# Optimization experiments

Measured on AMD Instinct MI355X. Metric: run time of the kernel, lower is better.

The kernel has to match this reference:

```python
import jax, jax.numpy as jnp
import numpy as np

B, S, E = 4, 1024, 1280
H = 16
D = E // H  # 80


def rotate_half(x):
    x1, x2 = jnp.split(x, 2, axis=-1)
    return jnp.concatenate([-x2, x1], axis=-1)


def setup_inputs() -> dict:
    key = jax.random.key(0)
    ks = jax.random.split(key, 12)
    sc = 0.02
    x = jax.random.normal(ks[0], (B, S, E), dtype=jnp.float32)
    # variable per-item sequence lengths (each <= S), cumulative
    lens = np.array([1024, 896, 768, 640], dtype=np.int32)
    cu_seqlens = jnp.asarray(np.concatenate([[0], np.cumsum(lens)]), dtype=jnp.int32)
    # rotary cos/sin for positions 0..S-1, head_dim D
    inv_freq = 1.0 / (10000.0 ** (np.arange(0, D, 2, dtype=np.float32) / D))
    t = np.arange(S, dtype=np.float32)
    freqs = np.outer(t, inv_freq)               # [S, D/2]
    emb = np.concatenate([freqs, freqs], axis=-1)  # [S, D]
    cos = jnp.asarray(np.cos(emb), dtype=jnp.float32)
    sin = jnp.asarray(np.sin(emb), dtype=jnp.float32)
    wq = jax.random.normal(ks[1], (E, E), dtype=jnp.float32) * sc
    bq = jax.random.normal(ks[2], (E,), dtype=jnp.float32) * sc
    wk = jax.random.normal(ks[3], (E, E), dtype=jnp.float32) * sc
    bk = jax.random.normal(ks[4], (E,), dtype=jnp.float32) * sc
    wv = jax.random.normal(ks[5], (E, E), dtype=jnp.float32) * sc
    bv = jax.random.normal(ks[6], (E,), dtype=jnp.float32) * sc
    wo = jax.random.normal(ks[7], (E, E), dtype=jnp.float32) * sc
    bo = jax.random.normal(ks[8], (E,), dtype=jnp.float32) * sc
    return {"x": x, "cu_seqlens": cu_seqlens, "cos": cos, "sin": sin,
            "wq": wq, "bq": bq, "wk": wk, "bk": bk, "wv": wv, "bv": bv,
            "wo": wo, "bo": bo}


def reference(x, cu_seqlens, cos, sin, wq, bq, wk, bk, wv, bv, wo, bo):
    b, s, e = x.shape
    h, d = H, D
    # QKV projections (nn.Linear: x @ W^T + b)
    q = (x @ wq.T + bq).reshape(b, s, h, d)
    k = (x @ wk.T + bk).reshape(b, s, h, d)
    v = (x @ wv.T + bv).reshape(b, s, h, d)
    # rotary embedding (apply_rotary_pos_emb, 'normal')
    c = cos[None, :, None, :]  # [1, s, 1, d]
    sn = sin[None, :, None, :]
    q = q * c + rotate_half(q) * sn
    k = k * c + rotate_half(k) * sn
    # patch attention mask from cu_seqlens (flatten_batch=False):
    # token i attends to token j iff i < len_b and j < len_b
    seq_lens = cu_seqlens[1:] - cu_seqlens[:-1]          # [b]
    idx = jnp.arange(s)
    valid = idx[None, :] < seq_lens[:, None]             # [b, s]
    mask = valid[:, None, :, None] & valid[:, None, None, :]  # [b, 1, s, s]
    # SDPA, non-causal
    scale = 1.0 / jnp.sqrt(jnp.asarray(d, dtype=q.dtype))
    scores = jnp.einsum("bqhd,bkhd->bhqk", q, k) * scale
    scores = jnp.where(mask, scores, jnp.asarray(-1e9, dtype=scores.dtype))
    attn = jax.nn.softmax(scores, axis=-1)
    out = jnp.einsum("bhqk,bkhd->bqhd", attn, v)         # [b, s, h, d]
    out = out.reshape(b, s, e)
    # output projection
    return out @ wo.T + bo
```

## Files before the change

### kernel.cpp

```cpp
#include <hip/hip_runtime.h>
#include <hip/hip_bf16.h>

#define B_ 4
#define S_ 1024
#define E_ 1280
#define H_ 16
#define D_ 80
#define M_ (B_*S_)

typedef __hip_bfloat16 bf16;
using bf16x8 = __attribute__((ext_vector_type(8))) short;
using f32x4  = __attribute__((ext_vector_type(4))) float;

__device__ __forceinline__ float b2f(bf16 x){ return __bfloat162float(x); }
__device__ __forceinline__ bf16  f2b(float x){ return __float2bfloat16(x); }
__device__ __forceinline__ void  stf(float* p, float v){ *p = v; }
__device__ __forceinline__ void  stf(bf16*  p, float v){ *p = f2b(v); }

__device__ __forceinline__ void gload_lds16(const void* g, void* l) {
    __builtin_amdgcn_global_load_lds(
        (const __attribute__((address_space(1))) unsigned int*)g,
        (__attribute__((address_space(3))) unsigned int*)l, 16, 0, 0);
}

__global__ __launch_bounds__(256) void cvt_kernel(
    const float* __restrict__ s0, const float* __restrict__ s1,
    const float* __restrict__ s2, const float* __restrict__ s3,
    const float* __restrict__ s4,
    bf16* __restrict__ d0, bf16* __restrict__ d1, bf16* __restrict__ d2,
    bf16* __restrict__ d3, bf16* __restrict__ d4,
    int n0, int n1)
{
    const float* s; bf16* d; int n;
    switch (blockIdx.y) {
        case 0: s = s0; d = d0; n = n0; break;
        case 1: s = s1; d = d1; n = n1; break;
        case 2: s = s2; d = d2; n = n1; break;
        case 3: s = s3; d = d3; n = n1; break;
        default: s = s4; d = d4; n = n1; break;
    }
    int i = (blockIdx.x * 256 + threadIdx.x) * 8;
    if (i >= n) return;
    float4 a = *(const float4*)(s + i);
    float4 b = *(const float4*)(s + i + 4);
    bf16 t[8];
    t[0]=f2b(a.x); t[1]=f2b(a.y); t[2]=f2b(a.z); t[3]=f2b(a.w);
    t[4]=f2b(b.x); t[5]=f2b(b.y); t[6]=f2b(b.z); t[7]=f2b(b.w);
    *(uint4*)(d + i) = *(const uint4*)t;
}

template<typename TC, bool VT_OUT>
__global__ __launch_bounds__(256) void mfma_gemm_bt(
    const bf16* __restrict__ A,
    const bf16* __restrict__ W0, const bf16* __restrict__ W1, const bf16* __restrict__ W2,
    const float* __restrict__ b0, const float* __restrict__ b1, const float* __restrict__ b2,
    TC* __restrict__ C0, TC* __restrict__ C1, TC* __restrict__ C2,
    int K, int N, int ntiles)
{
    const int mat = blockIdx.y / ntiles;
    const int bn  = (blockIdx.y % ntiles) * 128;
    const int bm  = blockIdx.x * 128;
    const bf16* W; const float* bias; TC* C;
    if (mat == 0)      { W = W0; bias = b0; C = C0; }
    else if (mat == 1) { W = W1; bias = b1; C = C1; }
    else               { W = W2; bias = b2; C = C2; }

    __shared__ bf16 As[2][128][32];
    __shared__ bf16 Ws[2][128][32];

    const int tid  = threadIdx.x;
    const int lane = tid & 63;
    const int wv   = tid >> 6;
    const int wm   = (wv & 1) * 64;
    const int wn   = (wv >> 1) * 64;
    const int srow = wv * 16 + (lane >> 2);
    const int scol = (lane & 3) * 8;

    f32x4 acc[4][4] = {};

    for (int k0 = 0; k0 < K; k0 += 64) {
        __syncthreads();
        #pragma unroll
        for (int p = 0; p < 2; p++) {
            const int kc = k0 + p*32 + scol;
            gload_lds16(A + (size_t)(bm + srow)      * K + kc, &As[p][wv*16][0]);
            gload_lds16(A + (size_t)(bm + 64 + srow) * K + kc, &As[p][64 + wv*16][0]);
            gload_lds16(W + (size_t)(bn + srow)      * K + kc, &Ws[p][wv*16][0]);
            gload_lds16(W + (size_t)(bn + 64 + srow) * K + kc, &Ws[p][64 + wv*16][0]);
        }
        __syncthreads();

        const int fr = lane & 15;
        const int kq = (lane >> 4) * 8;
        #pragma unroll
        for (int p = 0; p < 2; p++) {
            bf16x8 af[4], wf[4];
            #pragma unroll
            for (int t = 0; t < 4; t++) {
                af[t] = *(const bf16x8*)&As[p][wm + t*16 + fr][kq];
                wf[t] = *(const bf16x8*)&Ws[p][wn + t*16 + fr][kq];
            }
            #pragma unroll
            for (int mt = 0; mt < 4; mt++)
                #pragma unroll
                for (int nt = 0; nt < 4; nt++)
                    acc[mt][nt] = __builtin_amdgcn_mfma_f32_16x16x32_bf16(
                        af[mt], wf[nt], acc[mt][nt], 0, 0, 0);
        }
    }

    const int col_l = lane & 15;
    const int row_l = (lane >> 4) * 4;

    if (VT_OUT && mat == 2) {
        const int btok = bm >> 10;
        const int keyb = (bm & 1023) + wm + row_l;
        #pragma unroll
        for (int nt = 0; nt < 4; nt++) {
            const int n = bn + wn + nt*16 + col_l;
            const float bv = bias[n];
            const int hh = n / 80, dd = n % 80;
            bf16* vbase = (bf16*)C + ((size_t)(btok*H_ + hh)*D_ + dd)*S_ + keyb;
            #pragma unroll
            for (int mt = 0; mt < 4; mt++) {
                union { bf16 h[4]; uint2 u; } t4;
                #pragma unroll
                for (int r = 0; r < 4; r++) t4.h[r] = f2b(acc[mt][nt][r] + bv);
                *(uint2*)&vbase[mt*16] = t4.u;
            }
        }
    } else {
        #pragma unroll
        for (int nt = 0; nt < 4; nt++) {
            const int n = bn + wn + nt*16 + col_l;
            const float bv = bias[n];
            #pragma unroll
            for (int mt = 0; mt < 4; mt++) {
                #pragma unroll
                for (int r = 0; r < 4; r++) {
                    const int m = bm + wm + mt*16 + row_l + r;
                    stf(&C[(size_t)m * N + n], acc[mt][nt][r] + bv);
                }
            }
        }
    }
}

__device__ __forceinline__ void rope8(const bf16* lo, const bf16* hi,
                                      const float* cp, const float* sp,
                                      float mul, uint4* out_lo, uint4* out_hi)
{
    union { uint4 u; bf16 h[8]; } li, hi_, lo_o, hi_o;
    li.u  = *(const uint4*)lo;
    hi_.u = *(const uint4*)hi;
    #pragma unroll
    for (int u = 0; u < 8; u++) {
        float x1 = b2f(li.h[u]), x2 = b2f(hi_.h[u]);
        float c = cp[u], s = sp[u];
        lo_o.h[u] = f2b((x1*c - x2*s) * mul);
        hi_o.h[u] = f2b((x2*c + x1*s) * mul);
    }
    *out_lo = lo_o.u;
    *out_hi = hi_o.u;
}

__global__ __launch_bounds__(256) void rope_kernel(
    bf16* __restrict__ qp, bf16* __restrict__ kp,
    const float* __restrict__ cosp, const float* __restrict__ sinp)
{
    int idx = blockIdx.x * 256 + threadIdx.x;
    const int NT = M_ * H_ * 5;
    bf16* base; float mul;
    if (idx < NT) { base = qp; mul = 0.11180339887498949f; }
    else         { base = kp; mul = 1.0f; idx -= NT; }
    const int row = idx / 80;
    const int rem = idx - row * 80;
    const int h   = rem / 5;
    const int pc  = rem - h * 5;
    const int s   = row & (S_ - 1);
    bf16* p = base + (size_t)row * E_ + h * D_ + pc * 8;
    const float* cp = cosp + s * D_ + pc * 8;
    const float* sp = sinp + s * D_ + pc * 8;
    uint4 olo, ohi;
    rope8(p, p + 40, cp, sp, mul, &olo, &ohi);
    *(uint4*)p        = olo;
    *(uint4*)(p + 40) = ohi;
}

__global__ __launch_bounds__(256, 4) void attn_mfma(
    const bf16* __restrict__ q, const bf16* __restrict__ k, const bf16* __restrict__ vt,
    const int* __restrict__ cu, bf16* __restrict__ o)
{
    __shared__ __align__(16) bf16 Ks[64*80];
    __shared__ __align__(16) bf16 VTs[80*64];
    __shared__ __align__(16) bf16 PTs[4][16*76];

    const int n  = blockIdx.x;
    const int g  = (n & 7) * 8 + (n >> 7);
    const int qt = (n >> 3) & 15;
    const int b  = g >> 4;
    const int h  = g & 15;

    const int tid  = threadIdx.x;
    const int lane = tid & 63, wv = tid >> 6;
    const int quad = lane >> 4, l15 = lane & 15;
    const int q0   = qt * 64;
    const int len  = cu[b + 1] - cu[b];

    const bool uniformq = (q0 >= len);
    const bool cleanlen = ((len & 63) == 0);
    const int  ktiles   = uniformq ? 16 : (cleanlen ? (len >> 6) : 16);
    const bool domask   = !uniformq && !cleanlen;

    bf16* PT = &PTs[wv][0];

    bf16x8 qf[3] = {};
    if (!uniformq) {
        const bf16* qrow = q + (size_t)(b*S_ + q0 + wv*16 + l15)*E_ + h*D_ + quad*8;
        qf[0] = *(const bf16x8*)(qrow);
        qf[1] = *(const bf16x8*)(qrow + 32);
        if (quad < 2) qf[2] = *(const bf16x8*)(qrow + 64);
    } else {
        const bf16 one = f2b(1.0f);
        #pragma unroll
        for (int nt = 0; nt < 4; nt++)
            #pragma unroll
            for (int r = 0; r < 4; r++)
                PT[(quad*4 + r)*76 + nt*16 + l15] = one;
    }

    float m_r[4], l_r[4];
    #pragma unroll
    for (int r = 0; r < 4; r++) { m_r[r] = -1e30f; l_r[r] = 0.f; }
    f32x4 o_acc[5] = {};

    const bool q_full = (q0 + 64) <= len;

    const int u_  = l15 >> 2;
    const int s0r = quad ^ u_;
    const int sv0 = quad ^ (l15 & 7);

    for (int kt = 0; kt < ktiles; kt++) {
        __syncthreads();
        if (!uniformq) {
            #pragma unroll
            for (int i = 0; i < 3; i++) {
                int c = tid + i * 256;
                if (c < 640) {
                    int row = c / 10, s = c - row * 10;
                    int uu = (row >> 2) & 3;
                    int sg = (s < 8) ? (s ^ uu) : (8 + ((s ^ uu) & 1));
                    gload_lds16(k + (size_t)(b*S_ + kt*64 + row)*E_ + h*D_ + sg*8,
                                &Ks[c*8]);
                }
            }
        }
        #pragma unroll
        for (int i = 0; i < 3; i++) {
            int c = tid + i * 256;
            if (c < 640) {
                int row = c >> 3, s = c & 7;
                int sg = s ^ (row & 7);
                gload_lds16(vt + ((size_t)(b*H_ + h)*D_ + row)*S_ + kt*64 + sg*8,
                            &VTs[c*8]);
            }
        }
        __syncthreads();

        if (!uniformq) {
            f32x4 s4[4];
            #pragma unroll
            for (int nt = 0; nt < 4; nt++) {
                const bf16* kr = Ks + (nt*16 + l15) * 80;
                bf16x8 kf0 = *(const bf16x8*)(kr + s0r*8);
                bf16x8 kf1 = *(const bf16x8*)(kr + 32 + s0r*8);
                bf16x8 kf2 = {};
                if (quad < 2) kf2 = *(const bf16x8*)(kr + 64 + (s0r & 1)*8);
                f32x4 a0 = {};
                a0 = __builtin_amdgcn_mfma_f32_16x16x32_bf16(qf[0], kf0, a0, 0, 0, 0);
                a0 = __builtin_amdgcn_mfma_f32_16x16x32_bf16(qf[1], kf1, a0, 0, 0, 0);
                a0 = __builtin_amdgcn_mfma_f32_16x16x32_bf16(qf[2], kf2, a0, 0, 0, 0);
                s4[nt] = a0;
            }

            float sv[4][4];
            if (!domask || (q_full && (kt*64 + 64) <= len)) {
                #pragma unroll
                for (int r = 0; r < 4; r++)
                    #pragma unroll
                    for (int nt = 0; nt < 4; nt++)
                        sv[nt][r] = s4[nt][r];
            } else {
                bool vk[4];
                #pragma unroll
                for (int nt = 0; nt < 4; nt++) vk[nt] = (kt*64 + nt*16 + l15) < len;
                #pragma unroll
                for (int r = 0; r < 4; r++) {
                    const bool vq = (q0 + wv*16 + quad*4 + r) < len;
                    #pragma unroll
                    for (int nt = 0; nt < 4; nt++)
                        sv[nt][r] = (vq && vk[nt]) ? s4[nt][r] : -1e9f;
                }
            }
            float rmax[4];
            #pragma unroll
            for (int r = 0; r < 4; r++)
                rmax[r] = fmaxf(fmaxf(sv[0][r], sv[1][r]), fmaxf(sv[2][r], sv[3][r]));
            #pragma unroll
            for (int st = 1; st < 16; st <<= 1)
                #pragma unroll
                for (int r = 0; r < 4; r++)
                    rmax[r] = fmaxf(rmax[r], __shfl_xor(rmax[r], st, 64));
            float mnew[4], alpha[4], rsum[4], p[4][4];
            #pragma unroll
            for (int r = 0; r < 4; r++) {
                mnew[r]  = fmaxf(m_r[r], rmax[r]);
                alpha[r] = __expf(m_r[r] - mnew[r]);
                float a = 0.f;
                #pragma unroll
                for (int nt = 0; nt < 4; nt++) { p[nt][r] = __expf(sv[nt][r] - mnew[r]); a += p[nt][r]; }
                rsum[r] = a;
            }
            #pragma unroll
            for (int st = 1; st < 16; st <<= 1)
                #pragma unroll
                for (int r = 0; r < 4; r++)
                    rsum[r] += __shfl_xor(rsum[r], st, 64);
            #pragma unroll
            for (int r = 0; r < 4; r++) {
                l_r[r] = l_r[r] * alpha[r] + rsum[r];
                m_r[r] = mnew[r];
            }
            #pragma unroll
            for (int dt = 0; dt < 5; dt++)
                #pragma unroll
                for (int r = 0; r < 4; r++)
                    o_acc[dt][r] *= alpha[r];
            #pragma unroll
            for (int nt = 0; nt < 4; nt++)
                #pragma unroll
                for (int r = 0; r < 4; r++)
                    PT[(quad*4 + r)*76 + nt*16 + l15] = f2b(p[nt][r]);
        }

        bf16x8 pa0 = *(const bf16x8*)&PT[l15*76 + quad*8];
        bf16x8 pa1 = *(const bf16x8*)&PT[l15*76 + 32 + quad*8];
        #pragma unroll
        for (int dt = 0; dt < 5; dt++) {
            const bf16* vr = VTs + (dt*16 + l15) * 64;
            bf16x8 vf0 = *(const bf16x8*)(vr + sv0*8);
            bf16x8 vf1 = *(const bf16x8*)(vr + (sv0 ^ 4)*8);
            o_acc[dt] = __builtin_amdgcn_mfma_f32_16x16x32_bf16(pa0, vf0, o_acc[dt], 0, 0, 0);
            o_acc[dt] = __builtin_amdgcn_mfma_f32_16x16x32_bf16(pa1, vf1, o_acc[dt], 0, 0, 0);
        }
    }

    #pragma unroll
    for (int r = 0; r < 4; r++) {
        const float inv = uniformq ? (1.0f / 1024.0f) : (1.0f / l_r[r]);
        size_t row_g = (size_t)(b*S_ + q0 + wv*16 + quad*4 + r);
        #pragma unroll
        for (int dt = 0; dt < 5; dt++)
            o[row_g*E_ + h*D_ + dt*16 + l15] = f2b(o_acc[dt][r] * inv);
    }
}

extern "C" void kernel_launch(void* const* d_in, const int* in_sizes, int n_in,
                              void* d_out, int out_size, void* d_ws, size_t ws_size,
                              hipStream_t stream)
{
    const float* x    = (const float*)d_in[0];
    const int*   cu   = (const int*)  d_in[1];
    const float* cosp = (const float*)d_in[2];
    const float* sinp = (const float*)d_in[3];
    const float* wq   = (const float*)d_in[4];
    const float* bq   = (const float*)d_in[5];
    const float* wk   = (const float*)d_in[6];
    const float* bk   = (const float*)d_in[7];
    const float* wv   = (const float*)d_in[8];
    const float* bv   = (const float*)d_in[9];
    const float* wo   = (const float*)d_in[10];
    const float* bo   = (const float*)d_in[11];
    float* out = (float*)d_out;

    bf16* q   = (bf16*)d_ws;
    bf16* kk  = q   + (size_t)M_ * E_;
    bf16* vt  = kk  + (size_t)M_ * E_;
    bf16* ao  = vt  + (size_t)M_ * E_;
    bf16* xb  = ao  + (size_t)M_ * E_;
    bf16* wqb = xb  + (size_t)M_ * E_;
    bf16* wkb = wqb + (size_t)E_ * E_;
    bf16* wvb = wkb + (size_t)E_ * E_;
    bf16* wob = wvb + (size_t)E_ * E_;

    cvt_kernel<<<dim3(2560, 5), 256, 0, stream>>>(
        x, wq, wk, wv, wo, xb, wqb, wkb, wvb, wob, M_*E_, E_*E_);

    mfma_gemm_bt<bf16, true><<<dim3(M_/128, 30), 256, 0, stream>>>(
        xb, wqb, wkb, wvb, bq, bk, bv, q, kk, vt, E_, E_, 10);

    rope_kernel<<<2560, 256, 0, stream>>>(q, kk, cosp, sinp);

    attn_mfma<<<1024, 256, 0, stream>>>(q, kk, vt, cu, ao);

    mfma_gemm_bt<float, false><<<dim3(M_/128, 10), 256, 0, stream>>>(
        ao, wob, wob, wob, bo, bo, bo, out, out, out, E_, E_, 10);
}
```

Measured before the change: 280.6 us.

## Double-buffer K/V tiles and widen attention blocks to 128 queries

The attention kernel now handles 128 query rows per block with 8 waves instead of 64 rows with 4. This halves the number of K/V tile loads per (batch, head). K and V^T tiles are double-buffered in LDS, so the next tile is prefetched asynchronously while the current one is computed, and there is one barrier per iteration instead of two. LDS use per block doubles and the grid shrinks to 512 blocks, which lowers parallelism. The q_full check still uses a 64-row bound, so masking could be wrong for lengths that are not multiples of 128, though the test lengths are.

```diff
diff --git a/kernel.cpp b/kernel.cpp
--- a/kernel.cpp
+++ b/kernel.cpp
@@ -7,6 +7,7 @@
 #define H_ 16
 #define D_ 80
 #define M_ (B_*S_)
+#define QBLK 128
 
 typedef __hip_bfloat16 bf16;
 using bf16x8 = __attribute__((ext_vector_type(8))) short;
@@ -187,30 +188,30 @@
     *(uint4*)(p + 40) = ohi;
 }
 
-__global__ __launch_bounds__(256, 4) void attn_mfma(
+__global__ __launch_bounds__(512, 4) void attn_mfma(
     const bf16* __restrict__ q, const bf16* __restrict__ k, const bf16* __restrict__ vt,
     const int* __restrict__ cu, bf16* __restrict__ o)
 {
-    __shared__ __align__(16) bf16 Ks[64*80];
-    __shared__ __align__(16) bf16 VTs[80*64];
-    __shared__ __align__(16) bf16 PTs[4][16*76];
+    __shared__ __align__(16) bf16 Ks[2][64*80];
+    __shared__ __align__(16) bf16 VTs[2][80*64];
+    __shared__ __align__(16) bf16 PTs[8][16*76];
 
     const int n  = blockIdx.x;
-    const int g  = (n & 7) * 8 + (n >> 7);
-    const int qt = (n >> 3) & 15;
+    const int g  = ((n >> 6) << 3) | (n & 7);
+    const int qs = (n >> 3) & 7;
     const int b  = g >> 4;
     const int h  = g & 15;
 
     const int tid  = threadIdx.x;
     const int lane = tid & 63, wv = tid >> 6;
     const int quad = lane >> 4, l15 = lane & 15;
-    const int q0   = qt * 64;
+    const int q0   = qs * QBLK;
     const int len  = cu[b + 1] - cu[b];
 
     const bool uniformq = (q0 >= len);
-    const bool cleanlen = ((len & 63) == 0);
-    const int  ktiles   = uniformq ? 16 : (cleanlen ? (len >> 6) : 16);
-    const bool domask   = !uniformq && !cleanlen;
+    const bool clean    = ((len & (QBLK - 1)) == 0);
+    const int  ktiles   = uniformq ? 16 : (clean ? (len >> 6) : 16);
+    const bool domask   = !uniformq && !clean;
 
     bf16* PT = &PTs[wv][0];
 
@@ -234,44 +235,46 @@
     for (int r = 0; r < 4; r++) { m_r[r] = -1e30f; l_r[r] = 0.f; }
     f32x4 o_acc[5] = {};
 
-    const bool q_full = (q0 + 64) <= len;
-
     const int u_  = l15 >> 2;
     const int s0r = quad ^ u_;
     const int sv0 = quad ^ (l15 & 7);
 
+    auto stage = [&](int kt, int bf) {
+        #pragma unroll
+        for (int i = 0; i < 3; i++) {
+            int c = tid + i * 512;
+            if (c < 640) {
+                if (!uniformq) {
+                    int row = c / 10, s5 = c - row * 10;
+                    int uu = (row >> 2) & 3;
+                    int sg = (s5 < 8) ? (s5 ^ uu) : (8 + ((s5 ^ uu) & 1));
+                    gload_lds16(k + (size_t)(b*S_ + kt*64 + row)*E_ + h*D_ + sg*8,
+                                &Ks[bf][c*8]);
+                }
+            } else if (c < 1280) {
+                int c2 = c - 640;
+                int row = c2 >> 3, s5 = c2 & 7;
+                int sg = s5 ^ (row & 7);
+                gload_lds16(vt + ((size_t)(b*H_ + h)*D_ + row)*S_ + kt*64 + sg*8,
+                            &VTs[bf][c2*8]);
+            }
+        }
+    };
+
+    stage(0, 0);
+    __syncthreads();
+
+    const bool q_full = (q0 + 64) <= len;
+
     for (int kt = 0; kt < ktiles; kt++) {
-        __syncthreads();
-        if (!uniformq) {
-            #pragma unroll
-            for (int i = 0; i < 3; i++) {
-                int c = tid + i * 256;
-                if (c < 640) {
-                    int row = c / 10, s = c - row * 10;
-                    int uu = (row >> 2) & 3;
-                    int sg = (s < 8) ? (s ^ uu) : (8 + ((s ^ uu) & 1));
-                    gload_lds16(k + (size_t)(b*S_ + kt*64 + row)*E_ + h*D_ + sg*8,
-                                &Ks[c*8]);
-                }
-            }
-        }
-        #pragma unroll
-        for (int i = 0; i < 3; i++) {
-            int c = tid + i * 256;
-            if (c < 640) {
-                int row = c >> 3, s = c & 7;
-                int sg = s ^ (row & 7);
-                gload_lds16(vt + ((size_t)(b*H_ + h)*D_ + row)*S_ + kt*64 + sg*8,
-                            &VTs[c*8]);
-            }
-        }
-        __syncthreads();
+        const int cur = kt & 1;
+        if (kt + 1 < ktiles) stage(kt + 1, cur ^ 1);
 
         if (!uniformq) {
             f32x4 s4[4];
             #pragma unroll
             for (int nt = 0; nt < 4; nt++) {
-                const bf16* kr = Ks + (nt*16 + l15) * 80;
+                const bf16* kr = &Ks[cur][(nt*16 + l15) * 80];
                 bf16x8 kf0 = *(const bf16x8*)(kr + s0r*8);
                 bf16x8 kf1 = *(const bf16x8*)(kr + 32 + s0r*8);
                 bf16x8 kf2 = {};
@@ -347,12 +350,13 @@
         bf16x8 pa1 = *(const bf16x8*)&PT[l15*76 + 32 + quad*8];
         #pragma unroll
         for (int dt = 0; dt < 5; dt++) {
-            const bf16* vr = VTs + (dt*16 + l15) * 64;
+            const bf16* vr = &VTs[cur][(dt*16 + l15) * 64];
             bf16x8 vf0 = *(const bf16x8*)(vr + sv0*8);
             bf16x8 vf1 = *(const bf16x8*)(vr + (sv0 ^ 4)*8);
             o_acc[dt] = __builtin_amdgcn_mfma_f32_16x16x32_bf16(pa0, vf0, o_acc[dt], 0, 0, 0);
             o_acc[dt] = __builtin_amdgcn_mfma_f32_16x16x32_bf16(pa1, vf1, o_acc[dt], 0, 0, 0);
         }
+        __syncthreads();
     }
 
     #pragma unroll
@@ -401,7 +405,7 @@
 
     rope_kernel<<<2560, 256, 0, stream>>>(q, kk, cosp, sinp);
 
-    attn_mfma<<<1024, 256, 0, stream>>>(q, kk, vt, cu, ao);
+    attn_mfma<<<512, 512, 0, stream>>>(q, kk, vt, cu, ao);
 
     mfma_gemm_bt<float, false><<<dim3(M_/128, 10), 256, 0, stream>>>(
         ao, wob, wob, wob, bo, bo, bo, out, out, out, E_, E_, 10);
```

After: 269.2 us. 4.1% less time.
